# Kernel optimization log

Measured on AMD Instinct MI355X. Metric: run time of the kernel, lower is better.

The kernel has to match this reference:

```python
import math
import jax, jax.numpy as jnp
import numpy as np

INPUT_DIM = 1024
HEADS = 16
SEQ = 4096
BATCH = 1
SCALE = math.sqrt(INPUT_DIM / HEADS)  # 8.0


def setup_inputs() -> dict:
    key = jax.random.key(0)
    ks = jax.random.split(key, 5)
    D = INPUT_DIM
    return {
        "x": jax.random.normal(ks[0], (BATCH, SEQ, D), dtype=jnp.float32),
        "w_qkv": jax.random.normal(ks[1], (3 * D, D), dtype=jnp.float32) * (1.0 / math.sqrt(D)),
        "b_qkv": jax.random.normal(ks[2], (3 * D,), dtype=jnp.float32) * 0.01,
        "w_out": jax.random.normal(ks[3], (D, D), dtype=jnp.float32) * (1.0 / math.sqrt(D)),
        "b_out": jax.random.normal(ks[4], (D,), dtype=jnp.float32) * 0.01,
    }


def reference(x, w_qkv, b_qkv, w_out, b_out):
    b, n, D = x.shape
    h = HEADS
    d = D // h
    # qkv projection: [b, n, 3D]
    qkv = x @ w_qkv.T + b_qkv
    # 'b n (c h d) -> b c h n d' with c=3 outermost
    qkv = qkv.reshape(b, n, 3, h, d).transpose(2, 0, 3, 1, 4)  # [3, b, h, n, d]
    q, k, v = qkv[0], qkv[1], qkv[2]
    q = q / SCALE
    attn = jnp.einsum('bhnd,bhmd->bhnm', q, k)  # [b, h, n, n]
    attn = jax.nn.softmax(attn, axis=-1)
    # dropout is identity in eval mode
    context = jnp.einsum('bhnm,bhmd->bhnd', attn, v)  # [b, h, n, d]
    context = context.transpose(0, 2, 1, 3).reshape(b, n, D)  # 'b h n d -> b n (h d)'
    return context @ w_out.T + b_out
```

## Files before the change

kernel.cpp:

```cpp
#include <hip/hip_runtime.h>

typedef unsigned short u16;
typedef unsigned int u32;
typedef __attribute__((ext_vector_type(8))) short short8;
typedef __attribute__((ext_vector_type(4))) float f32x4;

__device__ __forceinline__ u16 f2b(float f) {
  union { float f; unsigned u; } v; v.f = f;
  unsigned r = (v.u + 0x7FFFu + ((v.u >> 16) & 1u)) >> 16;
  return (u16)r;
}
__device__ __forceinline__ float b2f(u16 b) {
  union { unsigned u; float f; } v; v.u = ((unsigned)b) << 16;
  return v.f;
}
__device__ __forceinline__ u32 cvtpk(float a, float b) {
  u32 r;
  asm("v_cvt_pk_bf16_f32 %0, %1, %2" : "=v"(r) : "v"(a), "v"(b));
  return r;
}
__device__ __forceinline__ void p32swap(u32& a, u32& b) {
  asm("v_permlane32_swap_b32 %0, %1" : "+v"(a), "+v"(b));
}
__device__ __forceinline__ void p16swap(u32& a, u32& b) {
  asm("v_permlane16_swap_b32 %0, %1" : "+v"(a), "+v"(b));
}
__device__ __forceinline__ float ldf(const void* p, size_t i, int f32) {
  return f32 ? ((const float*)p)[i] : b2f(((const u16*)p)[i]);
}

__global__ __launch_bounds__(256) void detect_dtype(const u16* __restrict__ x,
                                                    int* __restrict__ flag) {
  __shared__ int cnt;
  if (threadIdx.x == 0) cnt = 0;
  __syncthreads();
  int local = 0;
  for (int p = threadIdx.x; p < 512; p += 256) {
    int e = (x[2 * p] >> 7) & 0xFF;
    if (e >= 0xC0) local++;
  }
  atomicAdd(&cnt, local);
  __syncthreads();
  if (threadIdx.x == 0) flag[0] = (cnt >= 16) ? 1 : 0;
}

__global__ __launch_bounds__(256) void convert_all(
    const void* __restrict__ px, const void* __restrict__ pwq,
    const void* __restrict__ pbq, const void* __restrict__ pwo,
    const void* __restrict__ pbo, u16* __restrict__ xb,
    u16* __restrict__ wqkvb, u16* __restrict__ bqkvb, u16* __restrict__ wob,
    u16* __restrict__ bob) {
  __shared__ int sf;
  if (threadIdx.x == 0) sf = 0;
  __syncthreads();
  {
    const u16* xr = (const u16*)px;
    int local = 0;
    for (int p = threadIdx.x; p < 512; p += 256) {
      int e = (xr[2 * p] >> 7) & 0xFF;
      if (e >= 0xC0) local++;
    }
    atomicAdd(&sf, local);
  }
  __syncthreads();
  const int isf32 = (sf >= 16);

  int i = blockIdx.x * 256 + threadIdx.x;
  const void* in; u16* out; size_t g;
  if (i < 524288)       { in = px;  out = xb;    g = (size_t)i; }
  else if (i < 917504)  { in = pwq; out = wqkvb; g = (size_t)(i - 524288); }
  else if (i < 917888)  { in = pbq; out = bqkvb; g = (size_t)(i - 917504); }
  else if (i < 1048960) { in = pwo; out = wob;   g = (size_t)(i - 917888); }
  else                  { in = pbo; out = bob;   g = (size_t)(i - 1048960); }
  size_t base = g * 8;
  if (isf32) {
    const float* p = (const float*)in + base;
    float4 v0 = *(const float4*)p, v1 = *(const float4*)(p + 4);
    union { short8 v; u16 e[8]; } t;
    t.e[0]=f2b(v0.x); t.e[1]=f2b(v0.y); t.e[2]=f2b(v0.z); t.e[3]=f2b(v0.w);
    t.e[4]=f2b(v1.x); t.e[5]=f2b(v1.y); t.e[6]=f2b(v1.z); t.e[7]=f2b(v1.w);
    *(short8*)(out + base) = t.v;
  } else {
    *(short8*)(out + base) = *(const short8*)((const u16*)in + base);
  }
}

__global__ __launch_bounds__(256) void transpose_v(const u16* __restrict__ qkv,
                                                   u16* __restrict__ Vt) {
  __shared__ u16 T[64 * 72];
  const int tid = threadIdx.x;
  const int h = blockIdx.y;
  const int s0 = blockIdx.x * 64;
  for (int r = 0; r < 2; ++r) {
    int cid = r * 256 + tid;
    int s = cid >> 3, c8 = cid & 7;
    union { short8 v; u16 u[8]; } uu;
    uu.v = *(const short8*)(qkv + (size_t)(s0 + s) * 3072 + 2048 + h * 64 + c8 * 8);
    for (int i = 0; i < 8; ++i) T[(c8 * 8 + i) * 72 + s] = uu.u[i];
  }
  __syncthreads();
  for (int r = 0; r < 2; ++r) {
    int cid = r * 256 + tid;
    int dd = cid >> 3, c8 = cid & 7;
    union { short8 v; u16 u[8]; } uu;
    for (int i = 0; i < 8; ++i) uu.u[i] = T[dd * 72 + c8 * 8 + i];
    *(short8*)(Vt + (size_t)(h * 64 + dd) * 4096 + s0 + c8 * 8) = uu.v;
  }
}

__global__ __launch_bounds__(256) void gemm_bt(const void* __restrict__ A,
                                               const void* __restrict__ B,
                                               const void* __restrict__ bias,
                                               void* __restrict__ C,
                                               int M, int N, int K,
                                               int lda, int ldb, int ldc,
                                               int aMay, int bMay, int outF32,
                                               const int* __restrict__ flag) {
  __shared__ __align__(16) u16 sm[128 * 132];
  u16* As = sm;
  u16* Bs = sm + 128 * 64;
  const int f = flag[0];
  const int a32 = aMay && f, b32 = bMay && f;
  const int tid = threadIdx.x;
  const int w = tid >> 6, lane = tid & 63;
  const int lq = lane & 15, qr = lane >> 4;
  const int m0 = blockIdx.y * 128, n0 = blockIdx.x * 128;
  const int wm = (w >> 1) * 64, wn = (w & 1) * 64;

  f32x4 acc[4][4];
  for (int i = 0; i < 4; i++)
    for (int j = 0; j < 4; j++) acc[i][j] = (f32x4){0.f, 0.f, 0.f, 0.f};
  float bv[4];
  for (int ns = 0; ns < 4; ++ns) bv[ns] = ldf(bias, n0 + wn + ns * 16 + lq, b32);

  const int rs = tid >> 3, cs = tid & 7;
  const u16* gA = (const u16*)A + (size_t)(m0 + rs) * lda + cs * 8;
  const u16* gB = (const u16*)B + (size_t)(n0 + rs) * ldb + cs * 8;
  u16* lA = As + ((tid & ~63) << 3);
  u16* lB = Bs + ((tid & ~63) << 3);

  for (int k0 = 0; k0 < K; k0 += 64) {
    if (!(a32 | b32)) {
      for (int r = 0; r < 4; ++r) {
        __builtin_amdgcn_global_load_lds(gA + (size_t)(r * 32) * lda + k0,
                                         lA + r * 2048, 16, 0, 0);
        __builtin_amdgcn_global_load_lds(gB + (size_t)(r * 32) * ldb + k0,
                                         lB + r * 2048, 16, 0, 0);
      }
    } else {
      for (int r = 0; r < 4; ++r) {
        int cid = r * 256 + tid;
        int row = cid >> 3, c = cid & 7;
        if (a32) {
          const float* p = (const float*)A + (size_t)(m0 + row) * lda + k0 + c * 8;
          float4 v0 = *(const float4*)p, v1 = *(const float4*)(p + 4);
          union { short8 v; u16 e[8]; } t;
          t.e[0]=f2b(v0.x); t.e[1]=f2b(v0.y); t.e[2]=f2b(v0.z); t.e[3]=f2b(v0.w);
          t.e[4]=f2b(v1.x); t.e[5]=f2b(v1.y); t.e[6]=f2b(v1.z); t.e[7]=f2b(v1.w);
          *(short8*)(As + row * 64 + c * 8) = t.v;
        } else {
          *(short8*)(As + row * 64 + c * 8) =
              *(const short8*)((const u16*)A + (size_t)(m0 + row) * lda + k0 + c * 8);
        }
        if (b32) {
          const float* p = (const float*)B + (size_t)(n0 + row) * ldb + k0 + c * 8;
          float4 v0 = *(const float4*)p, v1 = *(const float4*)(p + 4);
          union { short8 v; u16 e[8]; } t;
          t.e[0]=f2b(v0.x); t.e[1]=f2b(v0.y); t.e[2]=f2b(v0.z); t.e[3]=f2b(v0.w);
          t.e[4]=f2b(v1.x); t.e[5]=f2b(v1.y); t.e[6]=f2b(v1.z); t.e[7]=f2b(v1.w);
          *(short8*)(Bs + row * 64 + c * 8) = t.v;
        } else {
          *(short8*)(Bs + row * 64 + c * 8) =
              *(const short8*)((const u16*)B + (size_t)(n0 + row) * ldb + k0 + c * 8);
        }
      }
    }
    __syncthreads();
    for (int ks = 0; ks < 2; ++ks) {
      short8 af[4], bf[4];
      const int sw = ks * 4 + qr;
      for (int i = 0; i < 4; i++) {
        af[i] = *(const short8*)(As + (wm + i * 16 + lq) * 64 + sw * 8);
        bf[i] = *(const short8*)(Bs + (wn + i * 16 + lq) * 64 + sw * 8);
      }
      for (int mi = 0; mi < 4; mi++)
        for (int ni = 0; ni < 4; ni++)
          acc[mi][ni] = __builtin_amdgcn_mfma_f32_16x16x32_bf16(
              af[mi], bf[ni], acc[mi][ni], 0, 0, 0);
    }
    __syncthreads();
  }

  if (!outF32) {
    u16* SH = sm;
    for (int mi = 0; mi < 4; mi++)
      for (int ni = 0; ni < 4; ni++)
        for (int r = 0; r < 4; ++r)
          SH[(wm + mi * 16 + qr * 4 + r) * 132 + wn + ni * 16 + lq] =
              f2b(acc[mi][ni][r] + bv[ni]);
    __syncthreads();
    for (int it = 0; it < 8; ++it) {
      int idx = it * 256 + tid;
      int row = idx >> 4, c8 = idx & 15;
      *(short8*)((u16*)C + (size_t)(m0 + row) * ldc + n0 + c8 * 8) =
          *(const short8*)(SH + row * 132 + c8 * 8);
    }
  } else {
    float* Cf = (float*)C;
    for (int mi = 0; mi < 4; mi++) {
      int row = m0 + wm + mi * 16 + qr * 4;
      for (int r = 0; r < 4; ++r) {
        float* rp = Cf + (size_t)(row + r) * ldc + n0 + wn;
        for (int ni = 0; ni < 4; ni++)
          rp[ni * 16 + lq] = acc[mi][ni][r] + bv[ni];
      }
    }
  }
}

__global__ __launch_bounds__(512, 2) void gemm_bt_ks(const u16* __restrict__ A,
                                                     const u16* __restrict__ B,
                                                     const u16* __restrict__ bias,
                                                     float* __restrict__ C,
                                                     int K, int lda, int ldb, int ldc) {
  __shared__ __align__(16) u16 sm[2][16384];
  const int tid = threadIdx.x;
  const int w = tid >> 6, lane = tid & 63;
  const int half = w >> 2, wq = w & 3;
  const int ht = tid & 255;
  const int lq = lane & 15, qr = lane >> 4;
  const int m0 = blockIdx.y * 128, n0 = blockIdx.x * 128;
  const int wm = (wq >> 1) * 64, wn = (wq & 1) * 64;
  const int kh = K >> 1;

  u16* As = &sm[half][0];
  u16* Bs = &sm[half][8192];

  f32x4 acc[4][4];
  for (int i = 0; i < 4; i++)
    for (int j = 0; j < 4; j++) acc[i][j] = (f32x4){0.f, 0.f, 0.f, 0.f};
  float bv[4];
  for (int ns = 0; ns < 4; ++ns) bv[ns] = b2f(bias[n0 + wn + ns * 16 + lq]);

  const int rs = ht >> 3, cs = ht & 7;
  const u16* gA = A + (size_t)(m0 + rs) * lda + half * kh + cs * 8;
  const u16* gB = B + (size_t)(n0 + rs) * ldb + half * kh + cs * 8;
  u16* lA = As + ((ht & ~63) << 3);
  u16* lB = Bs + ((ht & ~63) << 3);

  for (int k0 = 0; k0 < kh; k0 += 64) {
    for (int r = 0; r < 4; ++r) {
      __builtin_amdgcn_global_load_lds(gA + (size_t)(r * 32) * lda + k0,
                                       lA + r * 2048, 16, 0, 0);
      __builtin_amdgcn_global_load_lds(gB + (size_t)(r * 32) * ldb + k0,
                                       lB + r * 2048, 16, 0, 0);
    }
    __syncthreads();
    for (int ks = 0; ks < 2; ++ks) {
      short8 af[4], bf[4];
      const int sw = ks * 4 + qr;
      for (int i = 0; i < 4; i++) {
        af[i] = *(const short8*)(As + (wm + i * 16 + lq) * 64 + sw * 8);
        bf[i] = *(const short8*)(Bs + (wn + i * 16 + lq) * 64 + sw * 8);
      }
      for (int mi = 0; mi < 4; mi++)
        for (int ni = 0; ni < 4; ni++)
          acc[mi][ni] = __builtin_amdgcn_mfma_f32_16x16x32_bf16(
              af[mi], bf[ni], acc[mi][ni], 0, 0, 0);
    }
    __syncthreads();
  }

  float* CB = (float*)&sm[0][0];
  float* p = CB + (size_t)ht * 33;
  for (int t = 0; t < 2; ++t) {
    if (half == 1) {
      for (int u = 0; u < 2; ++u)
        for (int ni = 0; ni < 4; ++ni)
          for (int r = 0; r < 4; ++r)
            p[u * 16 + ni * 4 + r] = acc[2 * t + u][ni][r];
    }
    __syncthreads();
    if (half == 0) {
      for (int u = 0; u < 2; ++u)
        for (int ni = 0; ni < 4; ++ni)
          for (int r = 0; r < 4; ++r)
            acc[2 * t + u][ni][r] += p[u * 16 + ni * 4 + r];
    }
    __syncthreads();
  }

  if (half == 0) {
    for (int mi = 0; mi < 4; mi++) {
      int row = m0 + wm + mi * 16 + qr * 4;
      for (int r = 0; r < 4; ++r) {
        float* rp = C + (size_t)(row + r) * ldc + n0 + wn;
        for (int ni = 0; ni < 4; ni++)
          rp[ni * 16 + lq] = acc[mi][ni][r] + bv[ni];
      }
    }
  }
}

__global__ __launch_bounds__(512, 2) void attn_split(const u16* __restrict__ qkv,
                                                     const u16* __restrict__ Vtg,
                                                     u16* __restrict__ ctx, int ldctx) {
  __shared__ __align__(16) u16 SMEM[2][16384];
  const int tid = threadIdx.x;
  const int w = tid >> 6, lane = tid & 63;
  const int half = w >> 2, wq = w & 3, wl = w & 3;
  const int lq = lane & 15, qr = lane >> 4;
  const int qb = blockIdx.x, h = blockIdx.y;
  const int qbase = qb * 128 + wq * 32;
  const float cs = 0.18033688011112042f;

  short8 qf[2][2];
#pragma unroll
  for (int mi = 0; mi < 2; ++mi)
#pragma unroll
    for (int ks = 0; ks < 2; ++ks)
      qf[mi][ks] = *(const short8*)(qkv + (size_t)(qbase + mi * 16 + lq) * 3072 +
                                    h * 64 + ks * 32 + qr * 8);

  f32x4 o[2][4];
#pragma unroll
  for (int mi = 0; mi < 2; ++mi)
#pragma unroll
    for (int ds = 0; ds < 4; ++ds) o[mi][ds] = (f32x4){0.f, 0.f, 0.f, 0.f};
  float lrow[2] = {0.f, 0.f};

  const int csw = ((lane & 7) ^ (lane >> 3)) << 3;
  const int r0v = wl * 8 + (lane >> 3);
  const u16* sK0 = qkv + (size_t)(half * 2048 + r0v) * 3072 + 1024 + h * 64 + csw;
  const u16* sK1 = sK0 + (size_t)32 * 3072;
  const u16* sV0 = Vtg + (size_t)(h * 64 + r0v) * 4096 + half * 2048 + csw;
  const u16* sV1 = sV0 + (size_t)32 * 4096;
  const int kb = half * 4096 + wl * 512;
  const int vb = 8192 + half * 4096 + wl * 512;

#define STAGE(buf)                                                          \
  do {                                                                      \
    u16* B_ = &SMEM[buf][0];                                                \
    __builtin_amdgcn_global_load_lds(sK0, B_ + kb, 16, 0, 0);               \
    __builtin_amdgcn_global_load_lds(sK1, B_ + kb + 2048, 16, 0, 0);        \
    __builtin_amdgcn_global_load_lds(sV0, B_ + vb, 16, 0, 0);               \
    __builtin_amdgcn_global_load_lds(sV1, B_ + vb + 2048, 16, 0, 0);        \
    sK0 += (size_t)64 * 3072; sK1 += (size_t)64 * 3072;                     \
    sV0 += 64; sV1 += 64;                                                   \
  } while (0)

  STAGE(0);
  __syncthreads();

  for (int it = 0; it < 32; ++it) {
    const int cur = it & 1;
    if (it + 1 < 32) STAGE(cur ^ 1);
    const u16* Kh = &SMEM[cur][half * 4096];
    const u16* Vh = &SMEM[cur][8192 + half * 4096];

    f32x4 s[2][4];
#pragma unroll
    for (int mi = 0; mi < 2; ++mi)
#pragma unroll
      for (int ns = 0; ns < 4; ++ns) s[mi][ns] = (f32x4){0.f, 0.f, 0.f, 0.f};
#pragma unroll
    for (int ks = 0; ks < 2; ++ks) {
      short8 kf[4];
#pragma unroll
      for (int ns = 0; ns < 4; ++ns) {
        int rk = ns * 16 + lq;
        kf[ns] = *(const short8*)(Kh + rk * 64 + (((ks * 4 + qr) ^ (lq & 7)) << 3));
      }
      __builtin_amdgcn_s_setprio(1);
#pragma unroll
      for (int mi = 0; mi < 2; ++mi)
#pragma unroll
        for (int ns = 0; ns < 4; ++ns)
          s[mi][ns] = __builtin_amdgcn_mfma_f32_16x16x32_bf16(
              kf[ns], qf[mi][ks], s[mi][ns], 0, 0, 0);
      __builtin_amdgcn_s_setprio(0);
    }

    short8 pf[2][2];
#pragma unroll
    for (int mi = 0; mi < 2; ++mi) {
      float lacc = 0.f;
      u32 X[4], Y[4];
#pragma unroll
      for (int ns = 0; ns < 4; ++ns) {
        float p0 = __builtin_amdgcn_exp2f(fmaf(s[mi][ns][0], cs, -12.0f));
        float p1 = __builtin_amdgcn_exp2f(fmaf(s[mi][ns][1], cs, -12.0f));
        float p2 = __builtin_amdgcn_exp2f(fmaf(s[mi][ns][2], cs, -12.0f));
        float p3 = __builtin_amdgcn_exp2f(fmaf(s[mi][ns][3], cs, -12.0f));
        lacc += (p0 + p1) + (p2 + p3);
        X[ns] = cvtpk(p0, p1);
        Y[ns] = cvtpk(p2, p3);
      }
      lrow[mi] += lacc;
#pragma unroll
      for (int ks = 0; ks < 2; ++ks) {
        u32 a0 = X[2 * ks], b0 = X[2 * ks + 1];
        u32 a1 = Y[2 * ks], b1 = Y[2 * ks + 1];
        p32swap(a0, b0); p16swap(a0, b0);
        p32swap(a1, b1); p16swap(a1, b1);
        union { u32 u[4]; short8 v; } t;
        t.u[0] = a0; t.u[1] = a1; t.u[2] = b0; t.u[3] = b1;
        pf[mi][ks] = t.v;
      }
    }

#pragma unroll
    for (int ks = 0; ks < 2; ++ks) {
      short8 vf[4];
#pragma unroll
      for (int ds = 0; ds < 4; ++ds) {
        int dv = ds * 16 + lq;
        vf[ds] = *(const short8*)(Vh + (size_t)dv * 64 +
                                  (((ks * 4 + qr) ^ (lq & 7)) << 3));
      }
      __builtin_amdgcn_s_setprio(1);
#pragma unroll
      for (int mi = 0; mi < 2; ++mi)
#pragma unroll
        for (int ds = 0; ds < 4; ++ds)
          o[mi][ds] = __builtin_amdgcn_mfma_f32_16x16x32_bf16(
              vf[ds], pf[mi][ks], o[mi][ds], 0, 0, 0);
      __builtin_amdgcn_s_setprio(0);
    }
    __syncthreads();
  }
#undef STAGE

  float* CB = (float*)&SMEM[0][0];
#pragma unroll
  for (int mi = 0; mi < 2; ++mi) {
    float* p = CB + (size_t)(wq * 64 + lane) * 17;
    if (half == 1) {
#pragma unroll
      for (int ds = 0; ds < 4; ++ds) {
        p[ds * 4 + 0] = o[mi][ds][0];
        p[ds * 4 + 1] = o[mi][ds][1];
        p[ds * 4 + 2] = o[mi][ds][2];
        p[ds * 4 + 3] = o[mi][ds][3];
      }
      p[16] = lrow[mi];
    }
    __syncthreads();
    if (half == 0) {
#pragma unroll
      for (int ds = 0; ds < 4; ++ds) {
        o[mi][ds][0] += p[ds * 4 + 0];
        o[mi][ds][1] += p[ds * 4 + 1];
        o[mi][ds][2] += p[ds * 4 + 2];
        o[mi][ds][3] += p[ds * 4 + 3];
      }
      lrow[mi] += p[16];
    }
    __syncthreads();
  }

  if (half == 0) {
#pragma unroll
    for (int mi = 0; mi < 2; ++mi) {
      float l = lrow[mi];
      l += __shfl_xor(l, 16, 64);
      l += __shfl_xor(l, 32, 64);
      float linv = 1.f / fmaxf(l, 1e-30f);
      int row = qbase + mi * 16 + lq;
      u16* dst = ctx + (size_t)row * ldctx + h * 64 + qr * 4;
#pragma unroll
      for (int ds = 0; ds < 4; ++ds) {
        u32 lo = cvtpk(o[mi][ds][0] * linv, o[mi][ds][1] * linv);
        u32 hi = cvtpk(o[mi][ds][2] * linv, o[mi][ds][3] * linv);
        *(uint2*)(dst + ds * 16) = make_uint2(lo, hi);
      }
    }
  }
}

__global__ __launch_bounds__(256) void attn_fused(const u16* __restrict__ qkv,
                                                  const u16* __restrict__ Vtg,
                                                  u16* __restrict__ ctx, int ldctx) {
  __shared__ u16 Ks[64 * 64];
  __shared__ u16 Vts[64 * 64];
  const int tid = threadIdx.x;
  const int w = tid >> 6, lane = tid & 63;
  const int lq = lane & 15, qr = lane >> 4;
  const int qb = blockIdx.x, h = blockIdx.y;
  const int qbase = qb * 128 + w * 32;
  const float cs = 0.18033688011112042f;

  short8 qf[2][2];
  for (int mi = 0; mi < 2; ++mi)
    for (int ks = 0; ks < 2; ++ks)
      qf[mi][ks] = *(const short8*)(qkv + (size_t)(qbase + mi * 16 + lq) * 3072 +
                                    h * 64 + ks * 32 + qr * 8);

  f32x4 o[2][4];
  for (int mi = 0; mi < 2; ++mi)
    for (int ds = 0; ds < 4; ++ds) o[mi][ds] = (f32x4){0.f, 0.f, 0.f, 0.f};
  float lrow[2] = {0.f, 0.f};

  const int c = tid & 7, r0 = tid >> 3;
  u16* dKA = Ks + r0 * 64 + ((c ^ (r0 & 7)) << 3);
  u16* dKB = dKA + 32 * 64;
  const u16* sKA = qkv + (size_t)r0 * 3072 + 1024 + h * 64 + c * 8;
  const u16* sKB = sKA + (size_t)32 * 3072;
  const u16* sVfA = qkv + (size_t)r0 * 3072 + 2048 + h * 64 + c * 8;
  const u16* sVfB = sVfA + (size_t)32 * 3072;

  short8 rKA, rKB;
  union { short8 v; u16 e[8]; } ufA, ufB;
  rKA = *(const short8*)sKA; sKA += (size_t)64 * 3072;
  rKB = *(const short8*)sKB; sKB += (size_t)64 * 3072;
  ufA.v = *(const short8*)sVfA; sVfA += (size_t)64 * 3072;
  ufB.v = *(const short8*)sVfB; sVfB += (size_t)64 * 3072;

  for (int j0 = 0; j0 < 4096; j0 += 64) {
    __syncthreads();
    *(short8*)dKA = rKA;
    *(short8*)dKB = rKB;
    {
      const int jc = r0 >> 3;
      for (int i = 0; i < 8; ++i)
        Vts[(c * 8 + i) * 64 + ((jc ^ i) << 3) + (r0 & 7)] = ufA.e[i];
    }
    {
      const int jc = (r0 + 32) >> 3;
      for (int i = 0; i < 8; ++i)
        Vts[(c * 8 + i) * 64 + ((jc ^ i) << 3) + (r0 & 7)] = ufB.e[i];
    }
    __syncthreads();

    if (j0 + 64 < 4096) {
      rKA = *(const short8*)sKA; sKA += (size_t)64 * 3072;
      rKB = *(const short8*)sKB; sKB += (size_t)64 * 3072;
      ufA.v = *(const short8*)sVfA; sVfA += (size_t)64 * 3072;
      ufB.v = *(const short8*)sVfB; sVfB += (size_t)64 * 3072;
    }

    f32x4 s[2][4];
    for (int mi = 0; mi < 2; ++mi)
      for (int ns = 0; ns < 4; ++ns) s[mi][ns] = (f32x4){0.f, 0.f, 0.f, 0.f};
    for (int ks = 0; ks < 2; ++ks) {
      short8 kf[4];
      for (int ns = 0; ns < 4; ++ns) {
        int rk = ns * 16 + lq;
        kf[ns] = *(const short8*)(Ks + rk * 64 + (((ks * 4 + qr) ^ (lq & 7)) << 3));
      }
      __builtin_amdgcn_s_setprio(1);
      for (int mi = 0; mi < 2; ++mi)
        for (int ns = 0; ns < 4; ++ns)
          s[mi][ns] = __builtin_amdgcn_mfma_f32_16x16x32_bf16(
              kf[ns], qf[mi][ks], s[mi][ns], 0, 0, 0);
      __builtin_amdgcn_s_setprio(0);
    }

    short8 pf[2][2];
#pragma unroll
    for (int mi = 0; mi < 2; ++mi) {
      float lacc = 0.f;
      u32 X[4], Y[4];
#pragma unroll
      for (int ns = 0; ns < 4; ++ns) {
        float p0 = __builtin_amdgcn_exp2f(fmaf(s[mi][ns][0], cs, -12.0f));
        float p1 = __builtin_amdgcn_exp2f(fmaf(s[mi][ns][1], cs, -12.0f));
        float p2 = __builtin_amdgcn_exp2f(fmaf(s[mi][ns][2], cs, -12.0f));
        float p3 = __builtin_amdgcn_exp2f(fmaf(s[mi][ns][3], cs, -12.0f));
        lacc += (p0 + p1) + (p2 + p3);
        X[ns] = cvtpk(p0, p1);
        Y[ns] = cvtpk(p2, p3);
      }
      lrow[mi] += lacc;
#pragma unroll
      for (int ks = 0; ks < 2; ++ks) {
        u32 a0 = X[2 * ks], b0 = X[2 * ks + 1];
        u32 a1 = Y[2 * ks], b1 = Y[2 * ks + 1];
        p32swap(a0, b0); p16swap(a0, b0);
        p32swap(a1, b1); p16swap(a1, b1);
        union { u32 u[4]; short8 v; } t;
        t.u[0] = a0; t.u[1] = a1; t.u[2] = b0; t.u[3] = b1;
        pf[mi][ks] = t.v;
      }
    }

    for (int ks = 0; ks < 2; ++ks) {
      short8 vf[4];
      for (int ds = 0; ds < 4; ++ds) {
        int dv = ds * 16 + lq;
        vf[ds] = *(const short8*)(Vts + (size_t)dv * 64 +
                                  (((ks * 4 + qr) ^ (lq & 7)) << 3));
      }
      __builtin_amdgcn_s_setprio(1);
      for (int mi = 0; mi < 2; ++mi)
        for (int ds = 0; ds < 4; ++ds)
          o[mi][ds] = __builtin_amdgcn_mfma_f32_16x16x32_bf16(
              vf[ds], pf[mi][ks], o[mi][ds], 0, 0, 0);
      __builtin_amdgcn_s_setprio(0);
    }
  }

  for (int mi = 0; mi < 2; ++mi) {
    float l = lrow[mi];
    l += __shfl_xor(l, 16, 64);
    l += __shfl_xor(l, 32, 64);
    float linv = 1.f / fmaxf(l, 1e-30f);
    int row = qbase + mi * 16 + lq;
    u16* dst = ctx + (size_t)row * ldctx + h * 64 + qr * 4;
    for (int ds = 0; ds < 4; ++ds) {
      u32 lo = cvtpk(o[mi][ds][0] * linv, o[mi][ds][1] * linv);
      u32 hi = cvtpk(o[mi][ds][2] * linv, o[mi][ds][3] * linv);
      *(uint2*)(dst + ds * 16) = make_uint2(lo, hi);
    }
  }
}

extern "C" void kernel_launch(void* const* d_in, const int* in_sizes, int n_in,
                              void* d_out, int out_size, void* d_ws, size_t ws_size,
                              hipStream_t stream) {
  float* out = (float*)d_out;

  const void *px = nullptr, *pwq = nullptr, *pbq = nullptr, *pwo = nullptr, *pbo = nullptr;
  if (n_in == 5) {
    for (int i = 0; i < 5; ++i) {
      switch (in_sizes[i]) {
        case 4194304: px = d_in[i]; break;
        case 3145728: pwq = d_in[i]; break;
        case 3072:    pbq = d_in[i]; break;
        case 1048576: pwo = d_in[i]; break;
        case 1024:    pbo = d_in[i]; break;
        default: break;
      }
    }
  }
  if (!px || !pwq || !pbq || !pwo || !pbo) {
    px = d_in[0]; pwq = d_in[1]; pbq = d_in[2]; pwo = d_in[3]; pbo = d_in[4];
  }

  int* flag = (int*)d_ws;
  u16* qkv = (u16*)((char*)d_ws + 64);
  u16* ctx = qkv;

  const size_t nQKV = (size_t)4096 * 3072;
  const size_t nVt = (size_t)16 * 64 * 4096;
  const size_t nx = 4194304, nwq = 3145728, nwo = 1048576;
  u16* Vtg = qkv + nQKV;
  const size_t need_vt = 64 + (nQKV + nVt) * 2;
  const size_t need_full = need_vt + (nx + nwq + 4096 + nwo + 1024) * 2;

  if (ws_size >= need_full) {
    u16* xb    = Vtg + nVt;
    u16* wqkvb = xb + nx;
    u16* bqkvb = wqkvb + nwq;
    u16* wob   = bqkvb + 4096;
    u16* bob   = wob + nwo;
    convert_all<<<4098, 256, 0, stream>>>(px, pwq, pbq, pwo, pbo,
                                          xb, wqkvb, bqkvb, wob, bob);

    gemm_bt<<<dim3(24, 32), 256, 0, stream>>>(xb, wqkvb, bqkvb, qkv,
                                              4096, 3072, 1024, 1024, 1024, 3072,
                                              0, 0, 0, flag);
    transpose_v<<<dim3(64, 16), 256, 0, stream>>>(qkv, Vtg);
    attn_split<<<dim3(32, 16), 512, 0, stream>>>(qkv, Vtg, ctx, 3072);
    gemm_bt_ks<<<dim3(8, 32), 512, 0, stream>>>(ctx, wob, bob, out,
                                                1024, 3072, 1024, 1024);
  } else if (ws_size >= need_vt) {
    detect_dtype<<<1, 256, 0, stream>>>((const u16*)px, flag);
    gemm_bt<<<dim3(24, 32), 256, 0, stream>>>(px, pwq, pbq, qkv,
                                              4096, 3072, 1024, 1024, 1024, 3072,
                                              1, 1, 0, flag);
    transpose_v<<<dim3(64, 16), 256, 0, stream>>>(qkv, Vtg);
    attn_split<<<dim3(32, 16), 512, 0, stream>>>(qkv, Vtg, ctx, 3072);
    gemm_bt<<<dim3(8, 32), 256, 0, stream>>>(ctx, pwo, pbo, out,
                                             4096, 1024, 1024, 3072, 1024, 1024,
                                             0, 1, 1, flag);
  } else {
    detect_dtype<<<1, 256, 0, stream>>>((const u16*)px, flag);
    gemm_bt<<<dim3(24, 32), 256, 0, stream>>>(px, pwq, pbq, qkv,
                                              4096, 3072, 1024, 1024, 1024, 3072,
                                              1, 1, 0, flag);
    attn_fused<<<dim3(32, 16), 256, 0, stream>>>(qkv, (const u16*)nullptr, ctx, 3072);
    gemm_bt<<<dim3(8, 32), 256, 0, stream>>>(ctx, pwo, pbo, out,
                                             4096, 1024, 1024, 3072, 1024, 1024,
                                             0, 1, 1, flag);
  }
}
```

Before: 260.1 us.

## Add double-buffered direct-to-LDS GEMM kernel for QKV projection

Replaces the generic bf16 GEMM for the QKV projection with a specialised kernel. The new kernel stages A and B tiles straight from global memory into LDS with global_load_lds and double-buffers them, so the next K tile loads while MFMAs run on the current one. It also drops the runtime dtype-flag handling for this launch. The LDS tiles are unpadded 64-element rows, which risks bank conflicts on the 16-row fragment reads.

```diff
diff --git a/kernel.cpp b/kernel.cpp
--- a/kernel.cpp
+++ b/kernel.cpp
@@ -105,6 +105,81 @@
     union { short8 v; u16 u[8]; } uu;
     for (int i = 0; i < 8; ++i) uu.u[i] = T[dd * 72 + c8 * 8 + i];
     *(short8*)(Vt + (size_t)(h * 64 + dd) * 4096 + s0 + c8 * 8) = uu.v;
+  }
+}
+
+__global__ __launch_bounds__(256) void gemm1_db(const u16* __restrict__ A,
+                                                const u16* __restrict__ B,
+                                                const u16* __restrict__ bias,
+                                                u16* __restrict__ C,
+                                                int K, int lda, int ldb, int ldc) {
+  __shared__ __align__(16) u16 sm[2][16384];
+  const int tid = threadIdx.x;
+  const int w = tid >> 6, lane = tid & 63;
+  const int lq = lane & 15, qr = lane >> 4;
+  const int m0 = blockIdx.y * 128, n0 = blockIdx.x * 128;
+  const int wm = (w >> 1) * 64, wn = (w & 1) * 64;
+
+  f32x4 acc[4][4];
+  for (int i = 0; i < 4; i++)
+    for (int j = 0; j < 4; j++) acc[i][j] = (f32x4){0.f, 0.f, 0.f, 0.f};
+  float bv[4];
+  for (int ns = 0; ns < 4; ++ns) bv[ns] = b2f(bias[n0 + wn + ns * 16 + lq]);
+
+  const int rs = tid >> 3, cs = tid & 7;
+  const u16* gA = A + (size_t)(m0 + rs) * lda + cs * 8;
+  const u16* gB = B + (size_t)(n0 + rs) * ldb + cs * 8;
+  const int lofs = (tid & ~63) << 3;
+
+#define GSTAGE(buf, k0)                                                      \
+  do {                                                                       \
+    u16* As_ = &sm[buf][0];                                                  \
+    u16* Bs_ = &sm[buf][8192];                                               \
+    for (int r = 0; r < 4; ++r) {                                            \
+      __builtin_amdgcn_global_load_lds(gA + (size_t)(r * 32) * lda + (k0),   \
+                                       As_ + lofs + r * 2048, 16, 0, 0);     \
+      __builtin_amdgcn_global_load_lds(gB + (size_t)(r * 32) * ldb + (k0),   \
+                                       Bs_ + lofs + r * 2048, 16, 0, 0);     \
+    }                                                                        \
+  } while (0)
+
+  GSTAGE(0, 0);
+  __syncthreads();
+
+  const int nk = K >> 6;
+  for (int kt = 0; kt < nk; ++kt) {
+    const int cur = kt & 1;
+    if (kt + 1 < nk) GSTAGE(cur ^ 1, (kt + 1) * 64);
+    const u16* As = &sm[cur][0];
+    const u16* Bs = &sm[cur][8192];
+    for (int ks = 0; ks < 2; ++ks) {
+      short8 af[4], bf[4];
+      const int sw = ks * 4 + qr;
+      for (int i = 0; i < 4; i++) {
+        af[i] = *(const short8*)(As + (wm + i * 16 + lq) * 64 + sw * 8);
+        bf[i] = *(const short8*)(Bs + (wn + i * 16 + lq) * 64 + sw * 8);
+      }
+      for (int mi = 0; mi < 4; mi++)
+        for (int ni = 0; ni < 4; ni++)
+          acc[mi][ni] = __builtin_amdgcn_mfma_f32_16x16x32_bf16(
+              af[mi], bf[ni], acc[mi][ni], 0, 0, 0);
+    }
+    __syncthreads();
+  }
+#undef GSTAGE
+
+  u16* SH = &sm[0][0];
+  for (int mi = 0; mi < 4; mi++)
+    for (int ni = 0; ni < 4; ni++)
+      for (int r = 0; r < 4; ++r)
+        SH[(wm + mi * 16 + qr * 4 + r) * 132 + wn + ni * 16 + lq] =
+            f2b(acc[mi][ni][r] + bv[ni]);
+  __syncthreads();
+  for (int it = 0; it < 8; ++it) {
+    int idx = it * 256 + tid;
+    int row = idx >> 4, c8 = idx & 15;
+    *(short8*)(C + (size_t)(m0 + row) * ldc + n0 + c8 * 8) =
+        *(const short8*)(SH + row * 132 + c8 * 8);
   }
 }
 
@@ -657,9 +732,8 @@
     convert_all<<<4098, 256, 0, stream>>>(px, pwq, pbq, pwo, pbo,
                                           xb, wqkvb, bqkvb, wob, bob);
 
-    gemm_bt<<<dim3(24, 32), 256, 0, stream>>>(xb, wqkvb, bqkvb, qkv,
-                                              4096, 3072, 1024, 1024, 1024, 3072,
-                                              0, 0, 0, flag);
+    gemm1_db<<<dim3(24, 32), 256, 0, stream>>>(xb, wqkvb, bqkvb, qkv,
+                                               1024, 1024, 1024, 3072);
     transpose_v<<<dim3(64, 16), 256, 0, stream>>>(qkv, Vtg);
     attn_split<<<dim3(32, 16), 512, 0, stream>>>(qkv, Vtg, ctx, 3072);
     gemm_bt_ks<<<dim3(8, 32), 512, 0, stream>>>(ctx, wob, bob, out,
```

Result: faster. 244.6 us (-6.0%).
